# Kernel optimization log

Measured on AMD Instinct MI355X. Metric: run time of the kernel, lower is better.

## Reference

```python
import jax, jax.numpy as jnp
import numpy as np

N_MELS = 80
FORMANT_START, FORMANT_END = 10, 50
W_L1, W_DELTA, W_DELTA2, W_SC, W_BAND, FORMANT_W = 1.0, 0.5, 0.25, 0.5, 1.0, 2.0
EPS = 1e-8


def _masked_mean(x, mask):
    # mask broadcasts to x's shape; count = sum of the broadcast mask
    n = jnp.maximum(jnp.sum(jnp.broadcast_to(mask, x.shape)), 1.0)
    return jnp.sum(x * mask) / n


def setup_inputs() -> dict:
    key = jax.random.key(0)
    k1, k2, k3 = jax.random.split(key, 3)
    B, T, D = 64, 4000, N_MELS
    pred_mel = jax.random.normal(k1, (B, T, D), dtype=jnp.float32)
    target_mel = jax.random.normal(k2, (B, T, D), dtype=jnp.float32)
    lengths = jax.random.randint(k3, (B,), T // 2, T + 1)
    mel_mask = (jnp.arange(T)[None, :] < lengths[:, None]).astype(jnp.float32)
    band_weights = jnp.ones((D,), dtype=jnp.float32).at[FORMANT_START:FORMANT_END].set(FORMANT_W)
    return {"pred_mel": pred_mel, "target_mel": target_mel, "mel_mask": mel_mask,
            "band_weights": band_weights}


def reference(pred_mel, target_mel, mel_mask, band_weights):
    mask3 = mel_mask[:, :, None]                      # (B,T,1)

    l1 = jnp.abs(pred_mel - target_mel)               # (B,T,D)
    l1_loss = _masked_mean(l1, mask3)

    # 1st-order deltas
    dp = pred_mel[:, 1:] - pred_mel[:, :-1]
    dt = target_mel[:, 1:] - target_mel[:, :-1]
    dmask = (mel_mask[:, 1:] * mel_mask[:, :-1])[:, :, None]
    delta_loss = _masked_mean(jnp.abs(dp - dt), dmask)

    # 2nd-order deltas
    d2p = dp[:, 1:] - dp[:, :-1]
    d2t = dt[:, 1:] - dt[:, :-1]
    d2mask = (mel_mask[:, 2:] * mel_mask[:, 1:-1] * mel_mask[:, :-2])[:, :, None]
    delta2_loss = _masked_mean(jnp.abs(d2p - d2t), d2mask)

    # spectral convergence
    diff = (pred_mel - target_mel) * mask3
    tgt_m = target_mel * mask3
    n = jnp.maximum(jnp.sum(jnp.broadcast_to(mask3, pred_mel.shape)), 1.0)
    sc_num = jnp.sqrt(jnp.sum(diff * diff) / n)
    sc_den = jnp.maximum(jnp.sqrt(jnp.sum(tgt_m * tgt_m) / n), EPS)
    sc_loss = sc_num / sc_den

    # band-weighted L1
    w = band_weights[None, None, :]
    band_loss = _masked_mean(l1 * w, mask3) / jnp.mean(band_weights)

    # energy (per-frame mean over mel bins)
    e_l1 = jnp.abs(pred_mel.mean(axis=-1) - target_mel.mean(axis=-1))  # (B,T)
    energy_loss = _masked_mean(e_l1, mel_mask)

    return (W_L1 * l1_loss + W_DELTA * delta_loss + W_DELTA2 * delta2_loss
            + W_SC * sc_loss + W_BAND * band_loss + 0.5 * energy_loss)
```

## Files before the change

### kernel.cpp

```cpp
#include <hip/hip_runtime.h>
#include <math.h>

#define D_MELS 80
#define T_DIM  4000
#define NQ     10
#define NTHR   256
#define RPI    14


__global__ __launch_bounds__(NTHR, 8) void mel_loss_main(
    const float* __restrict__ pred, const float* __restrict__ tgt,
    const float* __restrict__ mask,
    float* __restrict__ partial, int BT, int Jtot, int nblk)
{
    const int tid  = threadIdx.x;
    const int lane = tid & 63;
    const int qtr  = lane & 3;
    const int rw   = lane >> 2;
    const int gw   = blockIdx.x * (NTHR / 64) + (tid >> 6);

    const float4* p4 = (const float4*)pred;
    const float4* q4 = (const float4*)tgt;
    const int lsrc4 = (lane - 4) & 63;
    const int lsrc8 = (lane - 8) & 63;

    float v_l1 = 0.f, v_band = 0.f, v_diff2 = 0.f, v_tgt2 = 0.f, v_energy = 0.f;
    float v_m = 0.f, v_d = 0.f, v_dm = 0.f, v_d2 = 0.f, v_d2m = 0.f;

    const int j0 = gw * 2;
    const int r0 = j0 * RPI - 2 + rw;

    int rl0 = r0 < 0 ? 0 : (r0 >= BT ? BT - 1 : r0);
    int rtmp = r0 + RPI;
    int rl1 = rtmp < 0 ? 0 : (rtmp >= BT ? BT - 1 : rtmp);
    float mv0 = (j0     < Jtot) ? mask[rl0] : 0.f;
    float mv1 = (j0 + 1 < Jtot) ? mask[rl1] : 0.f;

    #pragma unroll
    for (int s = 0; s < 2; ++s) {
        const int r = r0 + s * RPI;
        const float mload = s ? mv1 : mv0;

        if (!__any(mload != 0.0f)) continue;

        const int rload = r < 0 ? 0 : (r >= BT ? BT - 1 : r);
        const int t = rload % T_DIM;

        const float4* pr = p4 + (size_t)rload * (D_MELS / 4) + qtr;
        const float4* qr = q4 + (size_t)rload * (D_MELS / 4) + qtr;

        const float m1 = __shfl(mload, lsrc4, 64);
        const float m2 = __shfl(mload, lsrc8, 64);
        const bool contrib = (rw >= 2) && (r < BT);
        const float mt   = contrib ? mload : 0.f;
        const float dmv  = (t >= 1) ? mt * m1 : 0.f;
        const float d2mv = (t >= 2) ? dmv * m2 : 0.f;

        float l1r = 0.f, frr = 0.f, sqr = 0.f, t2r = 0.f, er = 0.f, dr = 0.f, d2r = 0.f;

        #pragma unroll 1
        for (int k = 0; k < 5; ++k) {
            float4 p = pr[4 * k];
            float4 q = qr[4 * k];
            float e0 = p.x - q.x, e1 = p.y - q.y, e2 = p.z - q.z, e3 = p.w - q.w;

            float f0 = __shfl(e0, lsrc4, 64);
            float f1 = __shfl(e1, lsrc4, 64);
            float f2 = __shfl(e2, lsrc4, 64);
            float f3 = __shfl(e3, lsrc4, 64);
            float g0 = __shfl(e0, lsrc8, 64);
            float g1 = __shfl(e1, lsrc8, 64);
            float g2 = __shfl(e2, lsrc8, 64);
            float g3 = __shfl(e3, lsrc8, 64);

            float a0 = fabsf(e0), a1 = fabsf(e1), a2 = fabsf(e2), a3 = fabsf(e3);
            l1r += a0 + a1 + a2 + a3;

            const int d0 = (k << 4) + (qtr << 2);
            frr += ((unsigned)(d0 + 0 - 10) < 40u ? a0 : 0.f)
                 + ((unsigned)(d0 + 1 - 10) < 40u ? a1 : 0.f)
                 + ((unsigned)(d0 + 2 - 10) < 40u ? a2 : 0.f)
                 + ((unsigned)(d0 + 3 - 10) < 40u ? a3 : 0.f);

            sqr += e0 * e0 + e1 * e1 + e2 * e2 + e3 * e3;
            t2r += q.x * q.x + q.y * q.y + q.z * q.z + q.w * q.w;
            er  += e0 + e1 + e2 + e3;
            dr  += fabsf(e0 - f0) + fabsf(e1 - f1) + fabsf(e2 - f2) + fabsf(e3 - f3);
            d2r += fabsf(e0 - 2.f * f0 + g0) + fabsf(e1 - 2.f * f1 + g1)
                 + fabsf(e2 - 2.f * f2 + g2) + fabsf(e3 - 2.f * f3 + g3);
        }

        v_l1    += l1r * mt;
        v_band  += (l1r + frr) * mt;
        v_diff2 += sqr * mt;
        v_tgt2  += t2r * mt;
        v_d     += dr * dmv;
        v_d2    += d2r * d2mv;

        er += __shfl_xor(er, 1, 64);
        er += __shfl_xor(er, 2, 64);
        if (qtr == 0) {
            v_energy += fabsf(er) * mt;
            v_m   += mt;
            v_dm  += dmv;
            v_d2m += d2mv;
        }
    }

    float vals[NQ] = {v_l1, v_band, v_diff2, v_tgt2, v_energy,
                      v_m, v_d, v_dm, v_d2, v_d2m};
    #pragma unroll
    for (int q = 0; q < NQ; ++q) {
        float v = vals[q];
        #pragma unroll
        for (int off = 32; off > 0; off >>= 1)
            v += __shfl_down(v, off, 64);
        vals[q] = v;
    }
    __shared__ float red[NTHR / 64][NQ];
    int wave = tid >> 6;
    if (lane == 0) {
        #pragma unroll
        for (int q = 0; q < NQ; ++q) red[wave][q] = vals[q];
    }
    __syncthreads();
    if (tid < NQ) {
        float s = 0.f;
        #pragma unroll
        for (int wv2 = 0; wv2 < NTHR / 64; ++wv2) s += red[wv2][tid];
        partial[tid * nblk + blockIdx.x] = s;
    }
}

__global__ __launch_bounds__(640) void mel_loss_finalize(
    const float* __restrict__ partial, const float* __restrict__ w,
    float* __restrict__ out, int nblk)
{
    const int tid = threadIdx.x;
    const int wv  = tid >> 6;
    const int lane = tid & 63;
    __shared__ float fin[NQ];

    float s = 0.f;
    for (int i = lane; i < nblk; i += 64) s += partial[wv * nblk + i];
    #pragma unroll
    for (int off = 32; off > 0; off >>= 1) s += __shfl_down(s, off, 64);
    if (lane == 0 && wv < NQ) fin[wv] = s;
    __syncthreads();

    if (tid == 0) {
        float l1s = fin[0], bands = fin[1], diff2 = fin[2], tgt2 = fin[3];
        float energys = fin[4], ms = fin[5], ds = fin[6], dms = fin[7];
        float d2s = fin[8], d2ms = fin[9];

        float wsum = 0.f;
        for (int d = 0; d < D_MELS; ++d) wsum += w[d];
        float wmean = wsum / (float)D_MELS;

        float n1  = fmaxf(ms   * (float)D_MELS, 1.f);
        float nd  = fmaxf(dms  * (float)D_MELS, 1.f);
        float nd2 = fmaxf(d2ms * (float)D_MELS, 1.f);

        float l1_loss     = l1s / n1;
        float delta_loss  = ds / nd;
        float delta2_loss = d2s / nd2;
        float sc_num = sqrtf(diff2 / n1);
        float sc_den = fmaxf(sqrtf(tgt2 / n1), 1e-8f);
        float sc_loss = sc_num / sc_den;
        float band_loss = (bands / n1) / wmean;
        float energy_loss = (energys / (float)D_MELS) / fmaxf(ms, 1.f);

        out[0] = 1.0f * l1_loss + 0.5f * delta_loss + 0.25f * delta2_loss
               + 0.5f * sc_loss + 1.0f * band_loss + 0.5f * energy_loss;
    }
}

extern "C" void kernel_launch(void* const* d_in, const int* in_sizes, int n_in,
                              void* d_out, int out_size, void* d_ws, size_t ws_size,
                              hipStream_t stream) {
    const float* pred = (const float*)d_in[0];
    const float* tgt  = (const float*)d_in[1];
    const float* mask = (const float*)d_in[2];
    const float* w    = (const float*)d_in[3];
    int BT = in_sizes[2];
    float* partial = (float*)d_ws;

    int Jtot = (BT + RPI - 1) / RPI;
    int nwaves = (Jtot + 1) / 2;
    int grid = (nwaves + (NTHR / 64) - 1) / (NTHR / 64);

    mel_loss_main<<<grid, NTHR, 0, stream>>>(pred, tgt, mask, partial, BT, Jtot, grid);
    mel_loss_finalize<<<1, 640, 0, stream>>>(partial, w, (float*)d_out, grid);
}
```

Before: 194.6 us.

## Stage error rows in LDS tiles instead of overlapping wave shuffles

Replaces the per-wave overlapping-row scheme, in which each 14-row item re-read 2 halo rows and used cross-lane shuffles for the deltas, with 64-row block tiles. Each tile is loaded cooperatively into LDS as pred-target differences plus a 2-row halo, and neighbouring rows are then read from LDS for the delta terms. This cuts redundant global loads of halo rows and the shuffle traffic. In exchange it adds LDS round trips and two block-wide barriers per tile, and lowers the launch-bounds occupancy hint. Loads for fully masked rows are skipped, and each block now handles two tiles in sequence.

```diff
diff --git a/kernel.cpp b/kernel.cpp
--- a/kernel.cpp
+++ b/kernel.cpp
@@ -2,108 +2,130 @@
 #include <math.h>
 
 #define D_MELS 80
+#define F4ROW  (D_MELS/4)
 #define T_DIM  4000
 #define NQ     10
 #define NTHR   256
-#define RPI    14
-
-
-__global__ __launch_bounds__(NTHR, 8) void mel_loss_main(
+#define RTILE  64
+#define EROWS  (RTILE + 2)
+#define EPITCH 84
+
+
+__global__ __launch_bounds__(NTHR, 4) void mel_loss_main(
     const float* __restrict__ pred, const float* __restrict__ tgt,
     const float* __restrict__ mask,
-    float* __restrict__ partial, int BT, int Jtot, int nblk)
+    float* __restrict__ partial, int BT, int ntiles, int TPB, int nblk)
 {
+    __shared__ float e_lds[EROWS * EPITCH];
+    __shared__ float smask[EROWS];
+    __shared__ float red[NTHR / 64][NQ];
+
     const int tid  = threadIdx.x;
     const int lane = tid & 63;
     const int qtr  = lane & 3;
     const int rw   = lane >> 2;
-    const int gw   = blockIdx.x * (NTHR / 64) + (tid >> 6);
+    const int wv   = tid >> 6;
 
     const float4* p4 = (const float4*)pred;
     const float4* q4 = (const float4*)tgt;
-    const int lsrc4 = (lane - 4) & 63;
-    const int lsrc8 = (lane - 8) & 63;
 
     float v_l1 = 0.f, v_band = 0.f, v_diff2 = 0.f, v_tgt2 = 0.f, v_energy = 0.f;
     float v_m = 0.f, v_d = 0.f, v_dm = 0.f, v_d2 = 0.f, v_d2m = 0.f;
 
-    const int j0 = gw * 2;
-    const int r0 = j0 * RPI - 2 + rw;
-
-    int rl0 = r0 < 0 ? 0 : (r0 >= BT ? BT - 1 : r0);
-    int rtmp = r0 + RPI;
-    int rl1 = rtmp < 0 ? 0 : (rtmp >= BT ? BT - 1 : rtmp);
-    float mv0 = (j0     < Jtot) ? mask[rl0] : 0.f;
-    float mv1 = (j0 + 1 < Jtot) ? mask[rl1] : 0.f;
-
-    #pragma unroll
-    for (int s = 0; s < 2; ++s) {
-        const int r = r0 + s * RPI;
-        const float mload = s ? mv1 : mv0;
-
-        if (!__any(mload != 0.0f)) continue;
-
-        const int rload = r < 0 ? 0 : (r >= BT ? BT - 1 : r);
-        const int t = rload % T_DIM;
-
-        const float4* pr = p4 + (size_t)rload * (D_MELS / 4) + qtr;
-        const float4* qr = q4 + (size_t)rload * (D_MELS / 4) + qtr;
-
-        const float m1 = __shfl(mload, lsrc4, 64);
-        const float m2 = __shfl(mload, lsrc8, 64);
-        const bool contrib = (rw >= 2) && (r < BT);
-        const float mt   = contrib ? mload : 0.f;
-        const float dmv  = (t >= 1) ? mt * m1 : 0.f;
-        const float d2mv = (t >= 2) ? dmv * m2 : 0.f;
-
-        float l1r = 0.f, frr = 0.f, sqr = 0.f, t2r = 0.f, er = 0.f, dr = 0.f, d2r = 0.f;
-
+    for (int it = 0; it < TPB; ++it) {
+        const int tile = blockIdx.x * TPB + it;
+        if (tile >= ntiles) break;
+        const int rbase = tile * RTILE;
+
+        if (it) __syncthreads();
+
+        if (tid < EROWS) {
+            int r = rbase - 2 + tid;
+            smask[tid] = (r >= 0 && r < BT) ? mask[r] : 0.f;
+        }
+        __syncthreads();
+
+        if (tid < 2 * F4ROW) {
+            int hr = tid / F4ROW;
+            int hc = tid % F4ROW;
+            int r  = rbase - 2 + hr;
+            float4 ev = make_float4(0.f, 0.f, 0.f, 0.f);
+            if (r >= 0 && r < BT && smask[hr] != 0.f) {
+                float4 p = p4[(size_t)r * F4ROW + hc];
+                float4 q = q4[(size_t)r * F4ROW + hc];
+                ev = make_float4(p.x - q.x, p.y - q.y, p.z - q.z, p.w - q.w);
+            }
+            ((float4*)&e_lds[hr * EPITCH])[hc] = ev;
+        }
         #pragma unroll 1
         for (int k = 0; k < 5; ++k) {
-            float4 p = pr[4 * k];
-            float4 q = qr[4 * k];
-            float e0 = p.x - q.x, e1 = p.y - q.y, e2 = p.z - q.z, e3 = p.w - q.w;
-
-            float f0 = __shfl(e0, lsrc4, 64);
-            float f1 = __shfl(e1, lsrc4, 64);
-            float f2 = __shfl(e2, lsrc4, 64);
-            float f3 = __shfl(e3, lsrc4, 64);
-            float g0 = __shfl(e0, lsrc8, 64);
-            float g1 = __shfl(e1, lsrc8, 64);
-            float g2 = __shfl(e2, lsrc8, 64);
-            float g3 = __shfl(e3, lsrc8, 64);
-
-            float a0 = fabsf(e0), a1 = fabsf(e1), a2 = fabsf(e2), a3 = fabsf(e3);
-            l1r += a0 + a1 + a2 + a3;
-
-            const int d0 = (k << 4) + (qtr << 2);
-            frr += ((unsigned)(d0 + 0 - 10) < 40u ? a0 : 0.f)
-                 + ((unsigned)(d0 + 1 - 10) < 40u ? a1 : 0.f)
-                 + ((unsigned)(d0 + 2 - 10) < 40u ? a2 : 0.f)
-                 + ((unsigned)(d0 + 3 - 10) < 40u ? a3 : 0.f);
-
-            sqr += e0 * e0 + e1 * e1 + e2 * e2 + e3 * e3;
-            t2r += q.x * q.x + q.y * q.y + q.z * q.z + q.w * q.w;
-            er  += e0 + e1 + e2 + e3;
-            dr  += fabsf(e0 - f0) + fabsf(e1 - f1) + fabsf(e2 - f2) + fabsf(e3 - f3);
-            d2r += fabsf(e0 - 2.f * f0 + g0) + fabsf(e1 - 2.f * f1 + g1)
-                 + fabsf(e2 - 2.f * f2 + g2) + fabsf(e3 - 2.f * f3 + g3);
-        }
-
-        v_l1    += l1r * mt;
-        v_band  += (l1r + frr) * mt;
-        v_diff2 += sqr * mt;
-        v_tgt2  += t2r * mt;
-        v_d     += dr * dmv;
-        v_d2    += d2r * d2mv;
-
-        er += __shfl_xor(er, 1, 64);
-        er += __shfl_xor(er, 2, 64);
-        if (qtr == 0) {
-            v_energy += fabsf(er) * mt;
-            v_m   += mt;
-            v_dm  += dmv;
-            v_d2m += d2mv;
+            int f4idx = tid + NTHR * k;
+            int row   = f4idx / F4ROW;
+            int col   = f4idx % F4ROW;
+            int r     = rbase + row;
+            float mval = smask[row + 2];
+            float4 ev = make_float4(0.f, 0.f, 0.f, 0.f);
+            if (r < BT && mval != 0.f) {
+                float4 p = p4[(size_t)r * F4ROW + col];
+                float4 q = q4[(size_t)r * F4ROW + col];
+                ev = make_float4(p.x - q.x, p.y - q.y, p.z - q.z, p.w - q.w);
+                v_tgt2 += (q.x * q.x + q.y * q.y + q.z * q.z + q.w * q.w) * mval;
+            }
+            ((float4*)&e_lds[(row + 2) * EPITCH])[col] = ev;
+        }
+        __syncthreads();
+
+        const int myrow = wv * 16 + rw;
+        const float m = smask[myrow + 2];
+        if (__any(m != 0.f)) {
+            const int r = rbase + myrow;
+            const float m1 = smask[myrow + 1];
+            const float m2 = smask[myrow];
+            const int t = r % T_DIM;
+            const float mt   = (r < BT) ? m : 0.f;
+            const float dmv  = (t >= 1) ? mt * m1 : 0.f;
+            const float d2mv = (t >= 2) ? dmv * m2 : 0.f;
+
+            const float4* e0p = (const float4*)&e_lds[(myrow + 2) * EPITCH];
+            const float4* e1p = (const float4*)&e_lds[(myrow + 1) * EPITCH];
+            const float4* e2p = (const float4*)&e_lds[(myrow    ) * EPITCH];
+
+            float l1r = 0.f, frr = 0.f, sqr = 0.f, er = 0.f, dr = 0.f, d2r = 0.f;
+            #pragma unroll 1
+            for (int k = 0; k < 5; ++k) {
+                float4 e = e0p[qtr + 4 * k];
+                float4 f = e1p[qtr + 4 * k];
+                float4 g = e2p[qtr + 4 * k];
+
+                float a0 = fabsf(e.x), a1 = fabsf(e.y), a2 = fabsf(e.z), a3 = fabsf(e.w);
+                l1r += a0 + a1 + a2 + a3;
+                const int d0 = (k << 4) + (qtr << 2);
+                frr += ((unsigned)(d0 + 0 - 10) < 40u ? a0 : 0.f)
+                     + ((unsigned)(d0 + 1 - 10) < 40u ? a1 : 0.f)
+                     + ((unsigned)(d0 + 2 - 10) < 40u ? a2 : 0.f)
+                     + ((unsigned)(d0 + 3 - 10) < 40u ? a3 : 0.f);
+                sqr += e.x * e.x + e.y * e.y + e.z * e.z + e.w * e.w;
+                er  += e.x + e.y + e.z + e.w;
+                dr  += fabsf(e.x - f.x) + fabsf(e.y - f.y)
+                     + fabsf(e.z - f.z) + fabsf(e.w - f.w);
+                d2r += fabsf(e.x - 2.f * f.x + g.x) + fabsf(e.y - 2.f * f.y + g.y)
+                     + fabsf(e.z - 2.f * f.z + g.z) + fabsf(e.w - 2.f * f.w + g.w);
+            }
+
+            v_l1    += l1r * mt;
+            v_band  += (l1r + frr) * mt;
+            v_diff2 += sqr * mt;
+            v_d     += dr * dmv;
+            v_d2    += d2r * d2mv;
+
+            er += __shfl_xor(er, 1, 64);
+            er += __shfl_xor(er, 2, 64);
+            if (qtr == 0) {
+                v_energy += fabsf(er) * mt;
+                v_m   += mt;
+                v_dm  += dmv;
+                v_d2m += d2mv;
+            }
         }
     }
 
@@ -117,11 +139,9 @@
             v += __shfl_down(v, off, 64);
         vals[q] = v;
     }
-    __shared__ float red[NTHR / 64][NQ];
-    int wave = tid >> 6;
     if (lane == 0) {
         #pragma unroll
-        for (int q = 0; q < NQ; ++q) red[wave][q] = vals[q];
+        for (int q = 0; q < NQ; ++q) red[wv][q] = vals[q];
     }
     __syncthreads();
     if (tid < NQ) {
@@ -185,10 +205,14 @@
     int BT = in_sizes[2];
     float* partial = (float*)d_ws;
 
-    int Jtot = (BT + RPI - 1) / RPI;
-    int nwaves = (Jtot + 1) / 2;
-    int grid = (nwaves + (NTHR / 64) - 1) / (NTHR / 64);
-
-    mel_loss_main<<<grid, NTHR, 0, stream>>>(pred, tgt, mask, partial, BT, Jtot, grid);
+    int ntiles = (BT + RTILE - 1) / RTILE;
+    int TPB = 2;
+    int grid = (ntiles + TPB - 1) / TPB;
+    while ((size_t)NQ * (size_t)grid * sizeof(float) > ws_size && TPB < ntiles) {
+        TPB *= 2;
+        grid = (ntiles + TPB - 1) / TPB;
+    }
+
+    mel_loss_main<<<grid, NTHR, 0, stream>>>(pred, tgt, mask, partial, BT, ntiles, TPB, grid);
     mel_loss_finalize<<<1, 640, 0, stream>>>(partial, w, (float*)d_out, grid);
 }
```

Measured after the change: 194.3 us. About the same (-0.1%).

## Precompute per-block mask flags and counts in a separate pre-pass kernel

Applied to the files above, without the earlier changes.

Adds a pre-pass kernel that reads only the mask, computes the mask/delta-mask counts and a per-block any-valid flag. The main kernel exits early for fully masked blocks and drops the count accumulators, which lowers the number of reductions. It also loads all five float4 pairs up front, before the wave-level skip check, to expose more memory parallelism. Per-wave row count K is chosen from workspace size (defaulting to 1), and occupancy is now 4 blocks per CU instead of 8. The cost is an extra kernel launch and loads that are no longer skipped for fully masked rows inside an active block.

```diff
diff --git a/kernel.cpp b/kernel.cpp
--- a/kernel.cpp
+++ b/kernel.cpp
@@ -2,53 +2,107 @@
 #include <math.h>
 
 #define D_MELS 80
+#define F4ROW  20
 #define T_DIM  4000
-#define NQ     10
+#define NQM    7
 #define NTHR   256
 #define RPI    14
 
-
-__global__ __launch_bounds__(NTHR, 8) void mel_loss_main(
-    const float* __restrict__ pred, const float* __restrict__ tgt,
-    const float* __restrict__ mask,
-    float* __restrict__ partial, int BT, int Jtot, int nblk)
+__global__ __launch_bounds__(NTHR) void mel_flags(
+    const float* __restrict__ mask, int* __restrict__ bflag,
+    float* __restrict__ cpart, int BT, int nmb, int rowsPerMB, int nfb)
 {
     const int tid  = threadIdx.x;
     const int lane = tid & 63;
+    const int wv   = tid >> 6;
+    const int g    = blockIdx.x * (NTHR / 64) + wv;
+
+    float cm = 0.f, cdm = 0.f, cd2m = 0.f;
+    int   fl = 0;
+
+    if (g < nmb) {
+        const int rlo = g * rowsPerMB;
+        int rhi = rlo + rowsPerMB; if (rhi > BT) rhi = BT;
+        for (int r = rlo - 2 + lane; r < rhi; r += 64) {
+            if (r < 0) continue;
+            float m = mask[r];
+            fl |= (m != 0.f);
+            if (r >= rlo && m != 0.f) {
+                int t = r % T_DIM;
+                cm += m;
+                if (t >= 1) {
+                    float m1 = mask[r - 1];
+                    cdm += m * m1;
+                    if (t >= 2) cd2m += m * m1 * mask[r - 2];
+                }
+            }
+        }
+    }
+
+    const bool anyl = __any(fl != 0);
+    #pragma unroll
+    for (int off = 32; off > 0; off >>= 1) {
+        cm   += __shfl_down(cm,   off, 64);
+        cdm  += __shfl_down(cdm,  off, 64);
+        cd2m += __shfl_down(cd2m, off, 64);
+    }
+    if (g < nmb && lane == 0) bflag[g] = anyl ? 1 : 0;
+
+    __shared__ float cred[NTHR / 64][3];
+    if (lane == 0) { cred[wv][0] = cm; cred[wv][1] = cdm; cred[wv][2] = cd2m; }
+    __syncthreads();
+    if (tid < 3) {
+        float s = 0.f;
+        #pragma unroll
+        for (int w2 = 0; w2 < NTHR / 64; ++w2) s += cred[w2][tid];
+        cpart[tid * nfb + blockIdx.x] = s;
+    }
+}
+
+__global__ __launch_bounds__(NTHR, 4) void mel_loss_main(
+    const float* __restrict__ pred, const float* __restrict__ tgt,
+    const float* __restrict__ mask, const int* __restrict__ bflag,
+    float* __restrict__ partial, int BT, int Jtot, int K, int nmb)
+{
+    const int tid = threadIdx.x;
+
+    if (!bflag[blockIdx.x]) {
+        if (tid < NQM) partial[tid * nmb + blockIdx.x] = 0.f;
+        return;
+    }
+
+    const int lane = tid & 63;
     const int qtr  = lane & 3;
     const int rw   = lane >> 2;
-    const int gw   = blockIdx.x * (NTHR / 64) + (tid >> 6);
+    const int wv   = tid >> 6;
+    const int gw   = blockIdx.x * (NTHR / 64) + wv;
 
     const float4* p4 = (const float4*)pred;
     const float4* q4 = (const float4*)tgt;
     const int lsrc4 = (lane - 4) & 63;
     const int lsrc8 = (lane - 8) & 63;
 
-    float v_l1 = 0.f, v_band = 0.f, v_diff2 = 0.f, v_tgt2 = 0.f, v_energy = 0.f;
-    float v_m = 0.f, v_d = 0.f, v_dm = 0.f, v_d2 = 0.f, v_d2m = 0.f;
-
-    const int j0 = gw * 2;
-    const int r0 = j0 * RPI - 2 + rw;
-
-    int rl0 = r0 < 0 ? 0 : (r0 >= BT ? BT - 1 : r0);
-    int rtmp = r0 + RPI;
-    int rl1 = rtmp < 0 ? 0 : (rtmp >= BT ? BT - 1 : rtmp);
-    float mv0 = (j0     < Jtot) ? mask[rl0] : 0.f;
-    float mv1 = (j0 + 1 < Jtot) ? mask[rl1] : 0.f;
-
-    #pragma unroll
-    for (int s = 0; s < 2; ++s) {
-        const int r = r0 + s * RPI;
-        const float mload = s ? mv1 : mv0;
+    float v_l1 = 0.f, v_frr = 0.f, v_diff2 = 0.f, v_tgt2 = 0.f, v_energy = 0.f;
+    float v_d = 0.f, v_d2 = 0.f;
+
+    const int j0 = gw * K;
+    for (int s = 0; s < K; ++s) {
+        const int j = j0 + s;
+        if (j >= Jtot) break;
+        const int r = j * RPI - 2 + rw;
+        const int rload = r < 0 ? 0 : (r >= BT ? BT - 1 : r);
+
+        const size_t rowb = (size_t)rload * F4ROW + qtr;
+        float  mload = mask[rload];
+        float4 P[5], Q[5];
+        #pragma unroll
+        for (int k = 0; k < 5; ++k) P[k] = p4[rowb + 4 * k];
+        #pragma unroll
+        for (int k = 0; k < 5; ++k) Q[k] = q4[rowb + 4 * k];
 
         if (!__any(mload != 0.0f)) continue;
 
-        const int rload = r < 0 ? 0 : (r >= BT ? BT - 1 : r);
         const int t = rload % T_DIM;
-
-        const float4* pr = p4 + (size_t)rload * (D_MELS / 4) + qtr;
-        const float4* qr = q4 + (size_t)rload * (D_MELS / 4) + qtr;
-
         const float m1 = __shfl(mload, lsrc4, 64);
         const float m2 = __shfl(mload, lsrc8, 64);
         const bool contrib = (rw >= 2) && (r < BT);
@@ -57,12 +111,10 @@
         const float d2mv = (t >= 2) ? dmv * m2 : 0.f;
 
         float l1r = 0.f, frr = 0.f, sqr = 0.f, t2r = 0.f, er = 0.f, dr = 0.f, d2r = 0.f;
-
-        #pragma unroll 1
+        #pragma unroll
         for (int k = 0; k < 5; ++k) {
-            float4 p = pr[4 * k];
-            float4 q = qr[4 * k];
-            float e0 = p.x - q.x, e1 = p.y - q.y, e2 = p.z - q.z, e3 = p.w - q.w;
+            float e0 = P[k].x - Q[k].x, e1 = P[k].y - Q[k].y,
+                  e2 = P[k].z - Q[k].z, e3 = P[k].w - Q[k].w;
 
             float f0 = __shfl(e0, lsrc4, 64);
             float f1 = __shfl(e1, lsrc4, 64);
@@ -75,15 +127,13 @@
 
             float a0 = fabsf(e0), a1 = fabsf(e1), a2 = fabsf(e2), a3 = fabsf(e3);
             l1r += a0 + a1 + a2 + a3;
-
             const int d0 = (k << 4) + (qtr << 2);
             frr += ((unsigned)(d0 + 0 - 10) < 40u ? a0 : 0.f)
                  + ((unsigned)(d0 + 1 - 10) < 40u ? a1 : 0.f)
                  + ((unsigned)(d0 + 2 - 10) < 40u ? a2 : 0.f)
                  + ((unsigned)(d0 + 3 - 10) < 40u ? a3 : 0.f);
-
             sqr += e0 * e0 + e1 * e1 + e2 * e2 + e3 * e3;
-            t2r += q.x * q.x + q.y * q.y + q.z * q.z + q.w * q.w;
+            t2r += Q[k].x * Q[k].x + Q[k].y * Q[k].y + Q[k].z * Q[k].z + Q[k].w * Q[k].w;
             er  += e0 + e1 + e2 + e3;
             dr  += fabsf(e0 - f0) + fabsf(e1 - f1) + fabsf(e2 - f2) + fabsf(e3 - f3);
             d2r += fabsf(e0 - 2.f * f0 + g0) + fabsf(e1 - 2.f * f1 + g1)
@@ -91,7 +141,7 @@
         }
 
         v_l1    += l1r * mt;
-        v_band  += (l1r + frr) * mt;
+        v_frr   += frr * mt;
         v_diff2 += sqr * mt;
         v_tgt2  += t2r * mt;
         v_d     += dr * dmv;
@@ -99,59 +149,56 @@
 
         er += __shfl_xor(er, 1, 64);
         er += __shfl_xor(er, 2, 64);
-        if (qtr == 0) {
-            v_energy += fabsf(er) * mt;
-            v_m   += mt;
-            v_dm  += dmv;
-            v_d2m += d2mv;
-        }
-    }
-
-    float vals[NQ] = {v_l1, v_band, v_diff2, v_tgt2, v_energy,
-                      v_m, v_d, v_dm, v_d2, v_d2m};
+        if (qtr == 0) v_energy += fabsf(er) * mt;
+    }
+
+    float vals[NQM] = {v_l1, v_frr, v_diff2, v_tgt2, v_energy, v_d, v_d2};
     #pragma unroll
-    for (int q = 0; q < NQ; ++q) {
+    for (int q = 0; q < NQM; ++q) {
         float v = vals[q];
         #pragma unroll
         for (int off = 32; off > 0; off >>= 1)
             v += __shfl_down(v, off, 64);
         vals[q] = v;
     }
-    __shared__ float red[NTHR / 64][NQ];
-    int wave = tid >> 6;
+    __shared__ float red[NTHR / 64][NQM];
     if (lane == 0) {
         #pragma unroll
-        for (int q = 0; q < NQ; ++q) red[wave][q] = vals[q];
+        for (int q = 0; q < NQM; ++q) red[wv][q] = vals[q];
     }
     __syncthreads();
-    if (tid < NQ) {
+    if (tid < NQM) {
         float s = 0.f;
         #pragma unroll
-        for (int wv2 = 0; wv2 < NTHR / 64; ++wv2) s += red[wv2][tid];
-        partial[tid * nblk + blockIdx.x] = s;
+        for (int w2 = 0; w2 < NTHR / 64; ++w2) s += red[w2][tid];
+        partial[tid * nmb + blockIdx.x] = s;
     }
 }
 
 __global__ __launch_bounds__(640) void mel_loss_finalize(
-    const float* __restrict__ partial, const float* __restrict__ w,
-    float* __restrict__ out, int nblk)
+    const float* __restrict__ partial, const float* __restrict__ cpart,
+    const float* __restrict__ w, float* __restrict__ out, int nmb, int nfb)
 {
     const int tid = threadIdx.x;
     const int wv  = tid >> 6;
     const int lane = tid & 63;
-    __shared__ float fin[NQ];
+    __shared__ float fin[10];
 
     float s = 0.f;
-    for (int i = lane; i < nblk; i += 64) s += partial[wv * nblk + i];
+    if (wv < NQM) {
+        for (int i = lane; i < nmb; i += 64) s += partial[wv * nmb + i];
+    } else {
+        for (int i = lane; i < nfb; i += 64) s += cpart[(wv - NQM) * nfb + i];
+    }
     #pragma unroll
     for (int off = 32; off > 0; off >>= 1) s += __shfl_down(s, off, 64);
-    if (lane == 0 && wv < NQ) fin[wv] = s;
+    if (lane == 0 && wv < 10) fin[wv] = s;
     __syncthreads();
 
     if (tid == 0) {
-        float l1s = fin[0], bands = fin[1], diff2 = fin[2], tgt2 = fin[3];
-        float energys = fin[4], ms = fin[5], ds = fin[6], dms = fin[7];
-        float d2s = fin[8], d2ms = fin[9];
+        float l1s = fin[0], frrs = fin[1], diff2 = fin[2], tgt2 = fin[3];
+        float energys = fin[4], ds = fin[5], d2s = fin[6];
+        float ms = fin[7], dms = fin[8], d2ms = fin[9];
 
         float wsum = 0.f;
         for (int d = 0; d < D_MELS; ++d) wsum += w[d];
@@ -167,7 +214,7 @@
         float sc_num = sqrtf(diff2 / n1);
         float sc_den = fmaxf(sqrtf(tgt2 / n1), 1e-8f);
         float sc_loss = sc_num / sc_den;
-        float band_loss = (bands / n1) / wmean;
+        float band_loss = ((l1s + frrs) / n1) / wmean;
         float energy_loss = (energys / (float)D_MELS) / fmaxf(ms, 1.f);
 
         out[0] = 1.0f * l1_loss + 0.5f * delta_loss + 0.25f * delta2_loss
@@ -183,12 +230,25 @@
     const float* mask = (const float*)d_in[2];
     const float* w    = (const float*)d_in[3];
     int BT = in_sizes[2];
+
+    int Jtot = (BT + RPI - 1) / RPI;
+
+    int K, nmb, nfb;
+    size_t need;
+    for (K = 1;; K *= 2) {
+        int nwaves = (Jtot + K - 1) / K;
+        nmb = (nwaves + (NTHR / 64) - 1) / (NTHR / 64);
+        nfb = (nmb + (NTHR / 64) - 1) / (NTHR / 64);
+        need = (size_t)(NQM * nmb + 3 * nfb) * sizeof(float) + (size_t)nmb * sizeof(int);
+        if (need <= ws_size || K >= Jtot) break;
+    }
+    const int rowsPerMB = (NTHR / 64) * K * RPI;
+
     float* partial = (float*)d_ws;
-
-    int Jtot = (BT + RPI - 1) / RPI;
-    int nwaves = (Jtot + 1) / 2;
-    int grid = (nwaves + (NTHR / 64) - 1) / (NTHR / 64);
-
-    mel_loss_main<<<grid, NTHR, 0, stream>>>(pred, tgt, mask, partial, BT, Jtot, grid);
-    mel_loss_finalize<<<1, 640, 0, stream>>>(partial, w, (float*)d_out, grid);
-}
+    float* cpart   = partial + NQM * nmb;
+    int*   bflag   = (int*)(cpart + 3 * nfb);
+
+    mel_flags<<<nfb, NTHR, 0, stream>>>(mask, bflag, cpart, BT, nmb, rowsPerMB, nfb);
+    mel_loss_main<<<nmb, NTHR, 0, stream>>>(pred, tgt, mask, bflag, partial, BT, Jtot, K, nmb);
+    mel_loss_finalize<<<1, 640, 0, stream>>>(partial, cpart, w, (float*)d_out, nmb, nfb);
+}
```

Measured after the change: 200.8 us. +3.2%, slower.
